# Kernel optimization log

Measured on AMD Instinct MI355X. Metric: run time of the kernel, lower is better.

The kernel has to match this reference:

```python
import jax, jax.numpy as jnp
import numpy as np

N = 100000
IN_C = 128
OUT_C = 200
E = 1600000


def gcn_conv(x, edge_index, W, b):
    """PyG GCNConv: symmetric degree-normalized aggregation with self-loops.
    out[v] = sum_{(u,v) in E+selfloops} d_u^-1/2 d_v^-1/2 (x_u @ W) + b
    """
    n = x.shape[0]
    xw = x @ W  # [N, out]
    loop = jnp.arange(n, dtype=edge_index.dtype)
    row = jnp.concatenate([edge_index[0], loop])  # src
    col = jnp.concatenate([edge_index[1], loop])  # dst
    ones = jnp.ones(row.shape[0], dtype=x.dtype)
    deg = jax.ops.segment_sum(ones, col, num_segments=n)  # in-degree incl. self
    dinv = jnp.where(deg > 0, jax.lax.rsqrt(deg), 0.0)
    norm = dinv[row] * dinv[col]  # [E+N]
    msgs = xw[row] * norm[:, None]  # [E+N, out]
    out = jax.ops.segment_sum(msgs, col, num_segments=n)
    return out + b


def setup_inputs() -> dict:
    key = jax.random.key(0)
    k1, k2, k3, k4 = jax.random.split(key, 4)
    x = jax.random.normal(k1, (N, IN_C), dtype=jnp.float32)
    edge_index = jax.random.randint(k2, (2, E), 0, N, dtype=jnp.int64)
    s1 = 1.0 / np.sqrt(IN_C)
    W1 = jax.random.uniform(k3, (IN_C, OUT_C), dtype=jnp.float32, minval=-s1, maxval=s1)
    b1 = jnp.zeros((OUT_C,), dtype=jnp.float32)
    W2 = jax.random.uniform(k4, (IN_C, OUT_C), dtype=jnp.float32, minval=-s1, maxval=s1)
    b2 = jnp.zeros((OUT_C,), dtype=jnp.float32)
    return {"x": x, "edge_index": edge_index, "W1": W1, "b1": b1, "W2": W2, "b2": b2}


def reference(x, edge_index, W1, b1, W2, b2):
    mu = gcn_conv(x, edge_index, W1, b1)
    logstd = gcn_conv(x, edge_index, W2, b2)
    return (mu, logstd)
```

## Files before the change

### kernel.cpp

```cpp
#include <hip/hip_runtime.h>

#define N_NODES 100000
#define IN_C    128
#define OUT_C   200
#define NT_TILES 13
#define KT_TILES 4

#define PSHIFT  8
#define NPB     256
#define NB      391
#define NB_POW2 512
#define BCAP    5120
#define PART_CH 4096

typedef __bf16 bf16_t;
typedef bf16_t bf16x8 __attribute__((ext_vector_type(8)));
typedef float  f32x4  __attribute__((ext_vector_type(4)));

__device__ __forceinline__ unsigned int bf16_bits(float f) {
    unsigned int u = __builtin_bit_cast(unsigned int, f);
    return (u + 0x7FFFu + ((u >> 16) & 1u)) >> 16;
}
__device__ __forceinline__ float bf16_lo(unsigned int p) {
    return __builtin_bit_cast(float, p << 16);
}
__device__ __forceinline__ float bf16_hi(unsigned int p) {
    return __builtin_bit_cast(float, p & 0xFFFF0000u);
}

__global__ __launch_bounds__(256) void partition_kernel(
        const int* __restrict__ row, const int* __restrict__ col, int E,
        int* __restrict__ gcount, unsigned int* __restrict__ gbuf) {
    __shared__ int hist[NB];
    __shared__ int base[NB];
    __shared__ int lofs[NB];
    __shared__ int pscan[256];
    __shared__ unsigned int stage[PART_CH];
    __shared__ unsigned short sb[PART_CH];
    const int tid = threadIdx.x;
    const int chunk = blockIdx.x * PART_CH;
    int cend = E - chunk; if (cend > PART_CH) cend = PART_CH;

    for (int i = tid; i < NB; i += 256) hist[i] = 0;
    __syncthreads();

    for (int i = tid; i < cend; i += 256) {
        int b = (col[chunk + i] >> PSHIFT) & (NB_POW2 - 1);
        if (b >= NB) b = NB - 1;
        atomicAdd(&hist[b], 1);
    }
    __syncthreads();

    for (int i = tid; i < NB; i += 256)
        base[i] = atomicAdd(&gcount[i], hist[i]);

    int v0 = (2 * tid     < NB) ? hist[2 * tid]     : 0;
    int v1 = (2 * tid + 1 < NB) ? hist[2 * tid + 1] : 0;
    int s = v0 + v1;
    pscan[tid] = s;
    __syncthreads();
    for (int off = 1; off < 256; off <<= 1) {
        int u = (tid >= off) ? pscan[tid - off] : 0;
        __syncthreads();
        pscan[tid] += u;
        __syncthreads();
    }
    int ep = pscan[tid] - s;
    if (2 * tid     < NB) lofs[2 * tid]     = ep;
    if (2 * tid + 1 < NB) lofs[2 * tid + 1] = ep + v0;
    __syncthreads();

    for (int i = tid; i < NB; i += 256) hist[i] = 0;
    __syncthreads();
    for (int i = tid; i < cend; i += 256) {
        int c = col[chunk + i];
        int r = row[chunk + i];
        int b = (c >> PSHIFT) & (NB_POW2 - 1);
        if (b >= NB) b = NB - 1;
        int p = lofs[b] + atomicAdd(&hist[b], 1);
        stage[p] = (unsigned int)((c & (NPB - 1)) | (r << PSHIFT));
        sb[p] = (unsigned short)b;
    }
    __syncthreads();

    for (int i = tid; i < cend; i += 256) {
        int b = sb[i];
        int p = base[b] + (i - lofs[b]);
        if (p < BCAP) gbuf[(size_t)b * BCAP + p] = stage[i];
    }
}

__global__ void bucket_scan_kernel(const int* __restrict__ gcount, int* __restrict__ gbase) {
    __shared__ int pscan[256];
    int tid = threadIdx.x;
    int v0 = (2 * tid     < NB) ? gcount[2 * tid]     : 0;
    int v1 = (2 * tid + 1 < NB) ? gcount[2 * tid + 1] : 0;
    if (v0 > BCAP) v0 = BCAP;
    if (v1 > BCAP) v1 = BCAP;
    int s = v0 + v1;
    pscan[tid] = s;
    __syncthreads();
    for (int off = 1; off < 256; off <<= 1) {
        int u = (tid >= off) ? pscan[tid - off] : 0;
        __syncthreads();
        pscan[tid] += u;
        __syncthreads();
    }
    int ep = pscan[tid] - s;
    if (2 * tid     < NB) gbase[2 * tid]     = ep;
    if (2 * tid + 1 < NB) gbase[2 * tid + 1] = ep + v0;
}

__global__ __launch_bounds__(256) void build_kernel(
        const unsigned int* __restrict__ gbuf, const int* __restrict__ gcount,
        const int* __restrict__ gbase, int* __restrict__ deg,
        int* __restrict__ offsets, float* __restrict__ dinv,
        int* __restrict__ csr_src, int n) {
    __shared__ int cnt[NPB];
    __shared__ int cur[NPB];
    __shared__ int pscan[256];
    const int b = blockIdx.x;
    const int tid = threadIdx.x;
    int total = gcount[b]; if (total > BCAP) total = BCAP;
    const int cbase = gbase[b];
    const unsigned int* bp = gbuf + (size_t)b * BCAP;

    cnt[tid] = 0;
    __syncthreads();
    for (int i = tid; i < total; i += 256)
        atomicAdd(&cnt[bp[i] & (NPB - 1)], 1);
    __syncthreads();

    int c = cnt[tid];
    pscan[tid] = c;
    __syncthreads();
    for (int off = 1; off < 256; off <<= 1) {
        int u = (tid >= off) ? pscan[tid - off] : 0;
        __syncthreads();
        pscan[tid] += u;
        __syncthreads();
    }
    int excl = pscan[tid] - c;
    cur[tid] = excl;
    int v = b * NPB + tid;
    if (v < n) {
        deg[v] = c;
        offsets[v] = cbase + excl;
        dinv[v] = rsqrtf((float)(c + 1));
    }
    __syncthreads();

    for (int i = tid; i < total; i += 256) {
        unsigned int e = bp[i];
        int p = atomicAdd(&cur[e & (NPB - 1)], 1);
        csr_src[cbase + p] = (int)(e >> PSHIFT);
    }
}

__global__ void convert_xs_kernel(const float4* __restrict__ x, const float* __restrict__ dinv,
                                  uint2* __restrict__ xs4, int n) {
    int id = blockIdx.x * blockDim.x + threadIdx.x;
    if (id >= n * 32) return;
    int v = id >> 5;
    float dv = dinv[v];
    float4 f = x[id];
    uint2 o;
    o.x = bf16_bits(f.x * dv) | (bf16_bits(f.y * dv) << 16);
    o.y = bf16_bits(f.z * dv) | (bf16_bits(f.w * dv) << 16);
    xs4[id] = o;
}

__global__ __launch_bounds__(256) void gather_kernel(
        const uint2* __restrict__ xs4, const float* __restrict__ dinv,
        const int* __restrict__ offsets, const int* __restrict__ deg,
        const int* __restrict__ csr_src, uint2* __restrict__ agg4, int n) {
    int wave = threadIdx.x >> 6;
    int lane = threadIdx.x & 63;
    int half = lane >> 5;
    int hl   = lane & 31;
    int v = blockIdx.x * 4 + wave;
    if (v >= n) return;
    float dv = dinv[v];
    int start = offsets[v];
    int cnt = deg[v];
    float ax = 0.f, ay = 0.f, az = 0.f, aw = 0.f;

    const int* cp = csr_src + start;
    int i = 0;
    for (; i + 16 <= cnt; i += 16) {
        int u[8];
        #pragma unroll
        for (int j = 0; j < 8; j++) u[j] = cp[i + 2 * j + half];
        uint2 t[8];
        #pragma unroll
        for (int j = 0; j < 8; j++) t[j] = xs4[(size_t)u[j] * 32 + hl];
        #pragma unroll
        for (int j = 0; j < 8; j++) {
            ax += bf16_lo(t[j].x); ay += bf16_hi(t[j].x);
            az += bf16_lo(t[j].y); aw += bf16_hi(t[j].y);
        }
    }
    for (; i + 2 <= cnt; i += 2) {
        int u = cp[i + half];
        uint2 t = xs4[(size_t)u * 32 + hl];
        ax += bf16_lo(t.x); ay += bf16_hi(t.x);
        az += bf16_lo(t.y); aw += bf16_hi(t.y);
    }
    if (i < cnt && half == 0) {
        int u = cp[i];
        uint2 t = xs4[(size_t)u * 32 + hl];
        ax += bf16_lo(t.x); ay += bf16_hi(t.x);
        az += bf16_lo(t.y); aw += bf16_hi(t.y);
    }
    ax += __shfl_xor(ax, 32, 64);
    ay += __shfl_xor(ay, 32, 64);
    az += __shfl_xor(az, 32, 64);
    aw += __shfl_xor(aw, 32, 64);
    uint2 s = xs4[(size_t)v * 32 + hl];
    ax += bf16_lo(s.x); ay += bf16_hi(s.x);
    az += bf16_lo(s.y); aw += bf16_hi(s.y);
    if (half == 0) {
        uint2 o;
        o.x = bf16_bits(ax * dv) | (bf16_bits(ay * dv) << 16);
        o.y = bf16_bits(az * dv) | (bf16_bits(aw * dv) << 16);
        agg4[(size_t)v * 32 + hl] = o;
    }
}

__global__ void pack_w_kernel(const float* __restrict__ W1, const float* __restrict__ W2,
                              unsigned short* __restrict__ out) {
    int tid = blockIdx.x * blockDim.x + threadIdx.x;
    if (tid >= 2 * KT_TILES * NT_TILES * 64) return;
    int lane = tid & 63;
    int nt = (tid >> 6) % NT_TILES;
    int kt = (tid / (64 * NT_TILES)) % KT_TILES;
    int h  = tid / (64 * NT_TILES * KT_TILES);
    const float* W = h ? W2 : W1;
    int q = lane >> 4, r = lane & 15;
    int nn = nt * 16 + r;
    size_t dst = ((size_t)((nt * 2 + h) * KT_TILES + kt)) * 512 + (size_t)lane * 8;
    for (int j = 0; j < 8; j++) {
        int k = kt * 32 + q * 8 + j;
        float val = (nn < OUT_C) ? W[(size_t)k * OUT_C + nn] : 0.f;
        out[dst + j] = (unsigned short)bf16_bits(val);
    }
}

__global__ __launch_bounds__(256) void gemm_mfma_kernel(
        const unsigned short* __restrict__ agg,
        const unsigned short* __restrict__ Wpk,
        const float* __restrict__ b1, const float* __restrict__ b2,
        float* __restrict__ mu, float* __restrict__ ls, int M) {
    __shared__ uint4 Bs[2][512];
    int tid  = threadIdx.x;
    int wave = tid >> 6;
    int lane = tid & 63;
    int row0 = blockIdx.x * 64 + wave * 16;
    int q = lane >> 4, r = lane & 15;

    int arow = row0 + r; if (arow > M - 1) arow = M - 1;
    const unsigned short* ap = agg + (size_t)arow * IN_C + q * 8;
    bf16x8 afrag[KT_TILES];
    #pragma unroll
    for (int kt = 0; kt < KT_TILES; kt++) {
        uint4 u = *(const uint4*)(ap + kt * 32);
        afrag[kt] = __builtin_bit_cast(bf16x8, u);
    }

    f32x4 acc[2][NT_TILES];
    #pragma unroll
    for (int h = 0; h < 2; h++)
        #pragma unroll
        for (int nt = 0; nt < NT_TILES; nt++)
            acc[h][nt] = (f32x4){0.f, 0.f, 0.f, 0.f};

    const uint4* wsrc = (const uint4*)Wpk;
    uint4 pre0 = wsrc[tid];
    uint4 pre1 = wsrc[tid + 256];

    for (int nt = 0; nt < NT_TILES; nt++) {
        int buf = nt & 1;
        Bs[buf][tid]       = pre0;
        Bs[buf][tid + 256] = pre1;
        __syncthreads();
        if (nt + 1 < NT_TILES) {
            pre0 = wsrc[(nt + 1) * 512 + tid];
            pre1 = wsrc[(nt + 1) * 512 + tid + 256];
        }
        #pragma unroll
        for (int h = 0; h < 2; h++) {
            f32x4 c = acc[h][nt];
            #pragma unroll
            for (int kt = 0; kt < KT_TILES; kt++) {
                uint4 u = Bs[buf][(h * KT_TILES + kt) * 64 + lane];
                bf16x8 bfrag = __builtin_bit_cast(bf16x8, u);
                c = __builtin_amdgcn_mfma_f32_16x16x32_bf16(afrag[kt], bfrag, c, 0, 0, 0);
            }
            acc[h][nt] = c;
        }
    }

    #pragma unroll
    for (int nt = 0; nt < NT_TILES; nt++) {
        int col = nt * 16 + r;
        bool cok = col < OUT_C;
        float bv1 = cok ? b1[col] : 0.f;
        float bv2 = cok ? b2[col] : 0.f;
        #pragma unroll
        for (int reg = 0; reg < 4; reg++) {
            int gr = row0 + q * 4 + reg;
            if (cok && gr < M) {
                mu[(size_t)gr * OUT_C + col] = acc[0][nt][reg] + bv1;
                ls[(size_t)gr * OUT_C + col] = acc[1][nt][reg] + bv2;
            }
        }
    }
}

extern "C" void kernel_launch(void* const* d_in, const int* in_sizes, int n_in,
                              void* d_out, int out_size, void* d_ws, size_t ws_size,
                              hipStream_t stream) {
    const float* x  = (const float*)d_in[0];
    const int*   ei = (const int*)d_in[1];
    const float* W1 = (const float*)d_in[2];
    const float* b1 = (const float*)d_in[3];
    const float* W2 = (const float*)d_in[4];
    const float* b2 = (const float*)d_in[5];

    const int n = in_sizes[0] / IN_C;
    const int E = in_sizes[1] / 2;
    const int* row = ei;
    const int* col = ei + E;

    float* mu = (float*)d_out;
    float* ls = (float*)d_out + (size_t)n * OUT_C;

    char* ws = (char*)d_ws;
    int*            deg     = (int*)           (ws + 0);
    float*          dinv    = (float*)         (ws + 524288);
    int*            offsets = (int*)           (ws + 1048576);
    int*            gcount  = (int*)           (ws + 1572864);
    int*            gbase   = (int*)           (ws + 1576960);
    int*            csr_src = (int*)           (ws + 2162688);
    unsigned int*   xs2     = (unsigned int*)  (ws + 8562688);
    unsigned int*   gbuf    = (unsigned int*)  (ws + 34162688);
    unsigned int*   agg2    = (unsigned int*)  (ws + 42170368);
    unsigned short* Wpk     = (unsigned short*)(ws + 67770368);

    hipMemsetAsync(gcount, 0, NB * sizeof(int), stream);

    pack_w_kernel<<<(2 * KT_TILES * NT_TILES * 64 + 255) / 256, 256, 0, stream>>>(W1, W2, Wpk);

    partition_kernel<<<(E + PART_CH - 1) / PART_CH, 256, 0, stream>>>(row, col, E, gcount, gbuf);
    bucket_scan_kernel<<<1, 256, 0, stream>>>(gcount, gbase);
    build_kernel<<<NB, 256, 0, stream>>>(gbuf, gcount, gbase, deg, offsets, dinv, csr_src, n);

    convert_xs_kernel<<<(n * 32 + 255) / 256, 256, 0, stream>>>(
        (const float4*)x, dinv, (uint2*)xs2, n);

    gather_kernel<<<(n + 3) / 4, 256, 0, stream>>>(
        (const uint2*)xs2, dinv, offsets, deg, csr_src, (uint2*)agg2, n);

    gemm_mfma_kernel<<<(n + 63) / 64, 256, 0, stream>>>(
        (const unsigned short*)agg2, Wpk, b1, b2, mu, ls, n);
}
```

Measured before the change: 428.5 us.

## Cache edge payloads in registers across partition and build passes, tune gather tail

Result: faster. 363.5 us (-15.2%).

```diff
diff --git a/kernel.cpp b/kernel.cpp
--- a/kernel.cpp
+++ b/kernel.cpp
@@ -12,6 +12,8 @@
 #define NB_POW2 512
 #define BCAP    5120
 #define PART_CH 4096
+#define SEQ_P   16
+#define SEQ_B   20
 
 typedef __bf16 bf16_t;
 typedef bf16_t bf16x8 __attribute__((ext_vector_type(8)));
@@ -44,10 +46,22 @@
     for (int i = tid; i < NB; i += 256) hist[i] = 0;
     __syncthreads();
 
-    for (int i = tid; i < cend; i += 256) {
-        int b = (col[chunk + i] >> PSHIFT) & (NB_POW2 - 1);
-        if (b >= NB) b = NB - 1;
-        atomicAdd(&hist[b], 1);
+    unsigned int   pay[SEQ_P];
+    unsigned short eb[SEQ_P];
+    unsigned short sq[SEQ_P];
+    #pragma unroll
+    for (int k = 0; k < SEQ_P; k++) {
+        int i = tid + k * 256;
+        eb[k] = 0xFFFFu;
+        if (i < cend) {
+            int c = col[chunk + i];
+            int r = row[chunk + i];
+            int b = (c >> PSHIFT) & (NB_POW2 - 1);
+            if (b >= NB) b = NB - 1;
+            pay[k] = (unsigned int)((c & (NPB - 1)) | (r << PSHIFT));
+            eb[k]  = (unsigned short)b;
+            sq[k]  = (unsigned short)atomicAdd(&hist[b], 1);
+        }
     }
     __syncthreads();
 
@@ -70,16 +84,13 @@
     if (2 * tid + 1 < NB) lofs[2 * tid + 1] = ep + v0;
     __syncthreads();
 
-    for (int i = tid; i < NB; i += 256) hist[i] = 0;
-    __syncthreads();
-    for (int i = tid; i < cend; i += 256) {
-        int c = col[chunk + i];
-        int r = row[chunk + i];
-        int b = (c >> PSHIFT) & (NB_POW2 - 1);
-        if (b >= NB) b = NB - 1;
-        int p = lofs[b] + atomicAdd(&hist[b], 1);
-        stage[p] = (unsigned int)((c & (NPB - 1)) | (r << PSHIFT));
-        sb[p] = (unsigned short)b;
+    #pragma unroll
+    for (int k = 0; k < SEQ_P; k++) {
+        if (eb[k] != 0xFFFFu) {
+            int p = lofs[eb[k]] + sq[k];
+            stage[p] = pay[k];
+            sb[p] = eb[k];
+        }
     }
     __syncthreads();
 
@@ -127,8 +138,19 @@
 
     cnt[tid] = 0;
     __syncthreads();
-    for (int i = tid; i < total; i += 256)
-        atomicAdd(&cnt[bp[i] & (NPB - 1)], 1);
+
+    unsigned int   ee[SEQ_B];
+    unsigned short sq[SEQ_B];
+    #pragma unroll
+    for (int k = 0; k < SEQ_B; k++) {
+        int i = tid + k * 256;
+        ee[k] = 0xFFFFFFFFu;
+        if (i < total) {
+            unsigned int e = bp[i];
+            ee[k] = e;
+            sq[k] = (unsigned short)atomicAdd(&cnt[e & (NPB - 1)], 1);
+        }
+    }
     __syncthreads();
 
     int c = cnt[tid];
@@ -150,10 +172,12 @@
     }
     __syncthreads();
 
-    for (int i = tid; i < total; i += 256) {
-        unsigned int e = bp[i];
-        int p = atomicAdd(&cur[e & (NPB - 1)], 1);
-        csr_src[cbase + p] = (int)(e >> PSHIFT);
+    #pragma unroll
+    for (int k = 0; k < SEQ_B; k++) {
+        if (ee[k] != 0xFFFFFFFFu) {
+            int p = cur[ee[k] & (NPB - 1)] + (int)sq[k];
+            csr_src[cbase + p] = (int)(ee[k] >> PSHIFT);
+        }
     }
 }
 
@@ -190,7 +214,7 @@
     for (; i + 16 <= cnt; i += 16) {
         int u[8];
         #pragma unroll
-        for (int j = 0; j < 8; j++) u[j] = cp[i + 2 * j + half];
+        for (int j = 0; j < 8; j++) u[j] = __builtin_nontemporal_load(cp + i + 2 * j + half);
         uint2 t[8];
         #pragma unroll
         for (int j = 0; j < 8; j++) t[j] = xs4[(size_t)u[j] * 32 + hl];
@@ -200,14 +224,43 @@
             az += bf16_lo(t[j].y); aw += bf16_hi(t[j].y);
         }
     }
-    for (; i + 2 <= cnt; i += 2) {
-        int u = cp[i + half];
+    if (i + 8 <= cnt) {
+        int u[4];
+        #pragma unroll
+        for (int j = 0; j < 4; j++) u[j] = __builtin_nontemporal_load(cp + i + 2 * j + half);
+        uint2 t[4];
+        #pragma unroll
+        for (int j = 0; j < 4; j++) t[j] = xs4[(size_t)u[j] * 32 + hl];
+        #pragma unroll
+        for (int j = 0; j < 4; j++) {
+            ax += bf16_lo(t[j].x); ay += bf16_hi(t[j].x);
+            az += bf16_lo(t[j].y); aw += bf16_hi(t[j].y);
+        }
+        i += 8;
+    }
+    if (i + 4 <= cnt) {
+        int u[2];
+        #pragma unroll
+        for (int j = 0; j < 2; j++) u[j] = __builtin_nontemporal_load(cp + i + 2 * j + half);
+        uint2 t[2];
+        #pragma unroll
+        for (int j = 0; j < 2; j++) t[j] = xs4[(size_t)u[j] * 32 + hl];
+        #pragma unroll
+        for (int j = 0; j < 2; j++) {
+            ax += bf16_lo(t[j].x); ay += bf16_hi(t[j].x);
+            az += bf16_lo(t[j].y); aw += bf16_hi(t[j].y);
+        }
+        i += 4;
+    }
+    if (i + 2 <= cnt) {
+        int u = __builtin_nontemporal_load(cp + i + half);
         uint2 t = xs4[(size_t)u * 32 + hl];
         ax += bf16_lo(t.x); ay += bf16_hi(t.x);
         az += bf16_lo(t.y); aw += bf16_hi(t.y);
+        i += 2;
     }
     if (i < cnt && half == 0) {
-        int u = cp[i];
+        int u = __builtin_nontemporal_load(cp + i);
         uint2 t = xs4[(size_t)u * 32 + hl];
         ax += bf16_lo(t.x); ay += bf16_hi(t.x);
         az += bf16_lo(t.y); aw += bf16_hi(t.y);
@@ -300,18 +353,29 @@
         }
     }
 
+    float bv1r[NT_TILES], bv2r[NT_TILES];
     #pragma unroll
     for (int nt = 0; nt < NT_TILES; nt++) {
-        int col = nt * 16 + r;
-        bool cok = col < OUT_C;
-        float bv1 = cok ? b1[col] : 0.f;
-        float bv2 = cok ? b2[col] : 0.f;
-        #pragma unroll
-        for (int reg = 0; reg < 4; reg++) {
-            int gr = row0 + q * 4 + reg;
-            if (cok && gr < M) {
-                mu[(size_t)gr * OUT_C + col] = acc[0][nt][reg] + bv1;
-                ls[(size_t)gr * OUT_C + col] = acc[1][nt][reg] + bv2;
+        int colx = nt * 16 + r;
+        bool cok = colx < OUT_C;
+        bv1r[nt] = cok ? b1[colx] : 0.f;
+        bv2r[nt] = cok ? b2[colx] : 0.f;
+    }
+    #pragma unroll
+    for (int reg = 0; reg < 4; reg++) {
+        int gr = row0 + q * 4 + reg;
+        if (gr < M) {
+            float* mrow = mu + (size_t)gr * OUT_C;
+            #pragma unroll
+            for (int nt = 0; nt < NT_TILES; nt++) {
+                int colx = nt * 16 + r;
+                if (colx < OUT_C) mrow[colx] = acc[0][nt][reg] + bv1r[nt];
+            }
+            float* lrow = ls + (size_t)gr * OUT_C;
+            #pragma unroll
+            for (int nt = 0; nt < NT_TILES; nt++) {
+                int colx = nt * 16 + r;
+                if (colx < OUT_C) lrow[colx] = acc[1][nt][reg] + bv2r[nt];
             }
         }
     }
```
